# Optimization experiments

Measured on AMD Instinct MI355X. Metric: run time of the kernel, lower is better.

Reference implementation:

```python
import jax, jax.numpy as jnp
import numpy as np

T, N, L_DIM, P_DIM = 8192, 4096, 64, 32
IN_DIM = 3 * L_DIM  # library = [identity, square, sin]
MIN_TEMP, ALPHA, REP_COEF = 0.01, 0.999, 0.1


def build_library(X):
    # (T, L) -> (T, 3L): concatenated library features
    return jnp.concatenate([X, X * X, jnp.sin(X)], axis=1)


def setup_inputs() -> dict:
    key = jax.random.key(0)
    k = jax.random.split(key, 8)
    u = jax.random.uniform(k[6], (P_DIM, IN_DIM), minval=1e-7, maxval=1.0)
    return {
        "X_tilde_t_batch": jax.random.normal(k[0], (T, L_DIM), jnp.float32),
        "X_train_t_batch": jax.random.normal(k[1], (T, N), jnp.float32),
        "Y_train_t_batch": jax.random.normal(k[2], (T, N), jnp.float32),
        "temp": jnp.ones((1,), jnp.float32),
        "phi_bar_t": jax.random.normal(k[3], (P_DIM, L_DIM), jnp.float32) * 0.01,
        # spectral radius ~0.9 so the 8192-step linear recurrence stays bounded
        "A_tilde": jax.random.normal(k[4], (L_DIM, L_DIM), jnp.float32) * (0.9 / np.sqrt(L_DIM)),
        "U_l": jax.random.normal(k[5], (N, L_DIM), jnp.float32) / np.sqrt(N),
        "logits": jax.random.normal(k[7], (P_DIM, IN_DIM), jnp.float32),
        "gumbel_g": -jnp.log(-jnp.log(u)),  # Gumbel(0,1) noise, precomputed
    }


def reference(X_tilde_t_batch, X_train_t_batch, Y_train_t_batch, temp,
              phi_bar_t, A_tilde, U_l, logits, gumbel_g):
    # --- GumbelSelector (train=True) ---
    X_mod = build_library(X_tilde_t_batch)                           # (T, 3L)
    new_temp = jnp.maximum(MIN_TEMP, temp[0] * ALPHA)
    soft = jax.nn.softmax((logits + gumbel_g) / new_temp, axis=-1)   # (P, 3L)
    X_sel = X_mod @ soft.T                                           # (T, P) -- computed but unused downstream, as in source
    selected_idx = jnp.argmax(logits, axis=-1)                       # (P,)
    probs = jax.nn.softmax(logits, axis=-1)
    l0_pen = REP_COEF * jnp.sum(jnp.max(probs, axis=-1))             # computed, unused (as in source)

    # --- reconstruction_error: sequential linear state-space recurrence ---
    x0 = X_train_t_batch[0]                                          # (N,)  first column of X_train_batch
    xh0 = U_l.T @ x0                                                 # (L,)  projected initial state
    phi_bar = phi_bar_t.T                                            # (L, P)

    def step(xh, _):
        mod_sel = jnp.take(xh, selected_idx, mode='clip')            # (P,) irregular gather (clip matches jit take)
        xh = A_tilde @ xh + phi_bar @ mod_sel                        # tiny matvecs
        return xh, xh

    _, xh_seq = jax.lax.scan(step, xh0, None, length=T)              # (T, L)
    X_rec = xh_seq @ U_l.T                                           # (T, N) == (U_r @ xh_seq.T).T with U_r = U_l
    # Frobenius norm is transpose-invariant, so compute in (T, N) layout
    err = jnp.linalg.norm(Y_train_t_batch - X_rec) / jnp.linalg.norm(Y_train_t_batch)
    return (X_rec, err, new_temp, selected_idx)
```

## Files before the change

### kernel.cpp

```cpp
#include <hip/hip_runtime.h>
#include <math.h>

#define T_DIM 8192
#define N_DIM 4096
#define L 64
#define P 32
#define IN_DIM 192
#define S_CHUNK 16
#define N_CHUNK (T_DIM / S_CHUNK)
#define LDST 68

using f32x4   = __attribute__((ext_vector_type(4))) float;
using bf16x8  = __attribute__((ext_vector_type(8))) short;
using ushort8 = __attribute__((ext_vector_type(8))) unsigned short;

__device__ __forceinline__ unsigned short f2bf(float x) {
  unsigned u = __float_as_uint(x);
  u += 0x7fffu + ((u >> 16) & 1u);
  return (unsigned short)(u >> 16);
}
__device__ __forceinline__ float bf2f(unsigned short h) {
  return __uint_as_float(((unsigned)h) << 16);
}

__global__ __launch_bounds__(64) void k_xh0_part(const float* __restrict__ U,
                                                 const float* __restrict__ Xtr,
                                                 float* __restrict__ part,
                                                 double* __restrict__ acc) {
  int b = blockIdx.x;
  int l = threadIdx.x;
  if (b == 0 && l < 2) acc[l] = 0.0;
  int n0 = b * 64;
  float s = 0.f;
  #pragma unroll 8
  for (int i = 0; i < 64; ++i) {
    float x = Xtr[n0 + i];
    s += U[(size_t)(n0 + i) * L + l] * x;
  }
  part[b * 64 + l] = s;
}

__global__ __launch_bounds__(256) void k_usplit(const float* __restrict__ U,
                                                unsigned short* __restrict__ uh,
                                                unsigned short* __restrict__ ul) {
  int i = blockIdx.x * 256 + threadIdx.x;
  float4 x = ((const float4*)U)[i];
  ushort4 h, lo;
  h.x = f2bf(x.x); lo.x = f2bf(x.x - bf2f(h.x));
  h.y = f2bf(x.y); lo.y = f2bf(x.y - bf2f(h.y));
  h.z = f2bf(x.z); lo.z = f2bf(x.z - bf2f(h.z));
  h.w = f2bf(x.w); lo.w = f2bf(x.w - bf2f(h.w));
  ((ushort4*)uh)[i] = h;
  ((ushort4*)ul)[i] = lo;
}

__global__ __launch_bounds__(256, 1) void k_prep(const float* __restrict__ A_tilde,
                                                 const float* __restrict__ phi_bar_t,
                                                 const float* __restrict__ logits,
                                                 const float* __restrict__ temp,
                                                 const float* __restrict__ part,
                                                 float* __restrict__ Wm,
                                                 float* __restrict__ xh0,
                                                 float* __restrict__ out_tail) {
  __shared__ float buf[2][64 * LDST];
  __shared__ float sphi[P * L];
  __shared__ float spart[4 * 64];
  __shared__ int   sel_s[P];
  int tid = threadIdx.x;

  #pragma unroll
  for (int i = 0; i < 4; ++i) {
    int f = tid + 256 * i;
    int r = f >> 4, q = f & 15;
    float4 v = ((const float4*)A_tilde)[f];
    *(float4*)(buf[0] + r * LDST + q * 4) = v;
  }
  #pragma unroll
  for (int i = 0; i < 2; ++i) {
    int f = tid + 256 * i;
    ((float4*)sphi)[f] = ((const float4*)phi_bar_t)[f];
  }
  {
    int l = tid & 63, q = tid >> 6;
    float s = 0.f;
    #pragma unroll
    for (int i = 0; i < 16; ++i)
      s += part[(q * 16 + i) * 64 + l];
    spart[q * 64 + l] = s;
  }
  {
    int p = tid >> 3, d = tid & 7;
    const float* row = logits + p * IN_DIM;
    float best = -1e30f; int bk = 0;
    #pragma unroll
    for (int j = 0; j < 6; ++j) {
      int kb = (j * 8 + d) * 4;
      float4 v = *(const float4*)(row + kb);
      if (v.x > best) { best = v.x; bk = kb; }
      if (v.y > best) { best = v.y; bk = kb + 1; }
      if (v.z > best) { best = v.z; bk = kb + 2; }
      if (v.w > best) { best = v.w; bk = kb + 3; }
    }
    #pragma unroll
    for (int off = 4; off > 0; off >>= 1) {
      float vo = __shfl_down(best, off, 8);
      int   ko = __shfl_down(bk,   off, 8);
      if (vo > best || (vo == best && ko < bk)) { best = vo; bk = ko; }
    }
    if (d == 0) {
      sel_s[p] = bk;
      out_tail[2 + p] = (float)bk;
    }
  }
  if (tid == 255) out_tail[1] = fmaxf(0.01f, temp[0] * 0.999f);
  __syncthreads();

  if (tid < L) {
    #pragma unroll 4
    for (int p = 0; p < P; ++p) {
      int kk = sel_s[p]; if (kk > L - 1) kk = L - 1;
      buf[0][tid * LDST + kk] += sphi[p * L + tid];
    }
  } else if (tid < 128) {
    int l = tid - 64;
    xh0[l] = spart[l] + spart[64 + l] + spart[128 + l] + spart[192 + l];
  }
  __syncthreads();

  #pragma unroll
  for (int i = 0; i < 4; ++i) {
    int f = tid + 256 * i;
    int r = f >> 4, q = f & 15;
    *(float4*)(Wm + r * 64 + q * 4) = *(const float4*)(buf[0] + r * LDST + q * 4);
  }

  int r0 = (tid >> 4) << 2;
  int c0 = (tid & 15) << 2;
  int cur = 0;
  for (int j = 1; j <= 12; ++j) {
    const float* S = buf[cur];
    float* D = buf[cur ^ 1];
    float acc[4][4];
    #pragma unroll
    for (int i = 0; i < 4; ++i)
      #pragma unroll
      for (int c = 0; c < 4; ++c) acc[i][c] = 0.f;

    #pragma unroll
    for (int kb = 0; kb < 64; kb += 16) {
      float a[4][16];
      #pragma unroll
      for (int i = 0; i < 4; ++i)
        #pragma unroll
        for (int q = 0; q < 4; ++q) {
          float4 t4 = *(const float4*)(S + (r0 + i) * LDST + kb + q * 4);
          a[i][q * 4 + 0] = t4.x; a[i][q * 4 + 1] = t4.y;
          a[i][q * 4 + 2] = t4.z; a[i][q * 4 + 3] = t4.w;
        }
      #pragma unroll
      for (int kk = 0; kk < 16; ++kk) {
        float4 b4 = *(const float4*)(S + (kb + kk) * LDST + c0);
        #pragma unroll
        for (int i = 0; i < 4; ++i) {
          acc[i][0] += a[i][kk] * b4.x;
          acc[i][1] += a[i][kk] * b4.y;
          acc[i][2] += a[i][kk] * b4.z;
          acc[i][3] += a[i][kk] * b4.w;
        }
      }
    }
    #pragma unroll
    for (int i = 0; i < 4; ++i) {
      float4 o = {acc[i][0], acc[i][1], acc[i][2], acc[i][3]};
      *(float4*)(D + (r0 + i) * LDST + c0) = o;
      *(float4*)(Wm + j * 4096 + (r0 + i) * 64 + c0) = o;
    }
    __syncthreads();
    cur ^= 1;
  }
}

__global__ __launch_bounds__(64) void k_states(const float* __restrict__ Wm,
                                               const float* __restrict__ xh0,
                                               unsigned short* __restrict__ xhi,
                                               unsigned short* __restrict__ xlo) {
  int c = blockIdx.x;
  int l = threadIdx.x;
  float v = xh0[l];
  int e = c << 4;
  for (int j = 4; j <= 12; ++j) {
    if ((e >> j) & 1) {
      const float* W = Wm + j * 4096;
      float n0 = 0.f, n1 = 0.f, n2 = 0.f, n3 = 0.f;
      #pragma unroll
      for (int k = 0; k < 64; k += 4) {
        n0 += W[l * 64 + k]     * __shfl(v, k, 64);
        n1 += W[l * 64 + k + 1] * __shfl(v, k + 1, 64);
        n2 += W[l * 64 + k + 2] * __shfl(v, k + 2, 64);
        n3 += W[l * 64 + k + 3] * __shfl(v, k + 3, 64);
      }
      v = (n0 + n1) + (n2 + n3);
    }
  }
  float m[64];
  #pragma unroll
  for (int k = 0; k < 64; ++k) m[k] = Wm[l * 64 + k];
  int t0 = c * S_CHUNK;
  for (int i = 0; i < S_CHUNK; ++i) {
    float n0 = 0.f, n1 = 0.f, n2 = 0.f, n3 = 0.f;
    #pragma unroll
    for (int k = 0; k < 64; k += 4) {
      n0 += m[k]     * __shfl(v, k, 64);
      n1 += m[k + 1] * __shfl(v, k + 1, 64);
      n2 += m[k + 2] * __shfl(v, k + 2, 64);
      n3 += m[k + 3] * __shfl(v, k + 3, 64);
    }
    v = (n0 + n1) + (n2 + n3);
    unsigned short h = f2bf(v);
    unsigned short lo = f2bf(v - bf2f(h));
    size_t base = (size_t)(t0 + i) * L + l;
    xhi[base] = h; xlo[base] = lo;
  }
}

__global__ __launch_bounds__(256, 2) void k_xrec(const unsigned short* __restrict__ xhi,
                                                 const unsigned short* __restrict__ xlo,
                                                 const unsigned short* __restrict__ uh,
                                                 const unsigned short* __restrict__ ul,
                                                 const float* __restrict__ Y,
                                                 float* __restrict__ Xrec,
                                                 double* __restrict__ acc_g) {
  __shared__ __align__(16) unsigned short Xs[128 * 128];
  __shared__ __align__(16) unsigned short Us[128 * 128];
  __shared__ float red[512];

  int tid = threadIdx.x;
  int nt = blockIdx.x & 31, tt = blockIdx.x >> 5;
  int n0 = nt * 128, t0 = tt * 128;

  #pragma unroll
  for (int i = 0; i < 8; ++i) {
    int c = tid + 256 * i;
    int t = c >> 4, p = c & 15;
    const ushort8* src = (p < 8)
      ? (const ushort8*)(xhi + (size_t)(t0 + t) * L + p * 8)
      : (const ushort8*)(xlo + (size_t)(t0 + t) * L + (p - 8) * 8);
    *(ushort8*)((char*)Xs + t * 256 + ((p * 16) ^ ((t & 7) << 4))) = *src;
  }
  #pragma unroll
  for (int i = 0; i < 8; ++i) {
    int c = tid + 256 * i;
    int nn = c >> 4, p = c & 15;
    const ushort8* src = (p < 8)
      ? (const ushort8*)(uh + (size_t)(n0 + nn) * L + p * 8)
      : (const ushort8*)(ul + (size_t)(n0 + nn) * L + (p - 8) * 8);
    *(ushort8*)((char*)Us + nn * 256 + ((p * 16) ^ ((nn & 7) << 4))) = *src;
  }
  __syncthreads();

  int l = tid & 63, wid = tid >> 6;
  int wr = wid >> 1, wc = wid & 1;
  int lr = l & 15, lg = l >> 4;

  f32x4 acc[4][4];
  #pragma unroll
  for (int m = 0; m < 4; ++m)
    #pragma unroll
    for (int nf = 0; nf < 4; ++nf) acc[m][nf] = (f32x4){0.f, 0.f, 0.f, 0.f};

  const int KA[6] = {0, 32, 64, 96, 0, 32};
  const int KB[6] = {0, 32, 0, 32, 64, 96};
  #pragma unroll
  for (int s = 0; s < 6; ++s) {
    bf16x8 af[4], bfr[4];
    #pragma unroll
    for (int m = 0; m < 4; ++m) {
      int t_loc = wr * 64 + m * 16 + lr;
      int kk = KA[s] + lg * 8;
      af[m] = *(const bf16x8*)((const char*)Xs + t_loc * 256 + ((kk * 2) ^ ((t_loc & 7) << 4)));
    }
    #pragma unroll
    for (int nf = 0; nf < 4; ++nf) {
      int n_loc = wc * 64 + nf * 16 + lr;
      int kk = KB[s] + lg * 8;
      bfr[nf] = *(const bf16x8*)((const char*)Us + n_loc * 256 + ((kk * 2) ^ ((n_loc & 7) << 4)));
    }
    #pragma unroll
    for (int m = 0; m < 4; ++m)
      #pragma unroll
      for (int nf = 0; nf < 4; ++nf)
        acc[m][nf] = __builtin_amdgcn_mfma_f32_16x16x32_bf16(bfr[nf], af[m], acc[m][nf], 0, 0, 0);
  }

  float sd = 0.f, sy = 0.f;
  #pragma unroll
  for (int m = 0; m < 4; ++m) {
    #pragma unroll
    for (int nf = 0; nf < 4; ++nf) {
      int t = t0 + wr * 64 + m * 16 + lr;
      int n = n0 + wc * 64 + nf * 16 + lg * 4;
      size_t idx = (size_t)t * N_DIM + n;
      float4 y = *(const float4*)(Y + idx);
      f32x4 v = acc[m][nf];
      float d;
      d = y.x - v[0]; sd += d * d; sy += y.x * y.x;
      d = y.y - v[1]; sd += d * d; sy += y.y * y.y;
      d = y.z - v[2]; sd += d * d; sy += y.z * y.z;
      d = y.w - v[3]; sd += d * d; sy += y.w * y.w;
      *(float4*)(Xrec + idx) = (float4){v[0], v[1], v[2], v[3]};
    }
  }

  red[tid] = sd; red[256 + tid] = sy;
  __syncthreads();
  for (int s2 = 128; s2 > 0; s2 >>= 1) {
    if (tid < s2) { red[tid] += red[tid + s2]; red[256 + tid] += red[256 + tid + s2]; }
    __syncthreads();
  }
  if (tid == 0) {
    atomicAdd(acc_g,     (double)red[0]);
    atomicAdd(acc_g + 1, (double)red[256]);
  }
}

__global__ void k_err(const double* __restrict__ acc, float* __restrict__ out_tail) {
  out_tail[0] = (float)sqrt(acc[0] / acc[1]);
}

extern "C" void kernel_launch(void* const* d_in, const int* in_sizes, int n_in,
                              void* d_out, int out_size, void* d_ws, size_t ws_size,
                              hipStream_t stream) {
  const float* X_train = (const float*)d_in[1];
  const float* Y       = (const float*)d_in[2];
  const float* temp    = (const float*)d_in[3];
  const float* phi     = (const float*)d_in[4];
  const float* A_tilde = (const float*)d_in[5];
  const float* U       = (const float*)d_in[6];
  const float* logits  = (const float*)d_in[7];
  float* out = (float*)d_out;
  float* out_tail = out + (size_t)T_DIM * N_DIM;

  char* w = (char*)d_ws;
  double* acc          = (double*)w;
  float* Wm            = (float*)(w + 64);
  float* xh0           = (float*)(w + 213056);
  float* part          = (float*)(w + 213312);
  unsigned short* uh   = (unsigned short*)(w + 262144);
  unsigned short* ul   = (unsigned short*)(w + 786432);
  unsigned short* xhi  = (unsigned short*)(w + 1310720);
  unsigned short* xlo  = (unsigned short*)(w + 2359296);

  k_xh0_part<<<64, 64, 0, stream>>>(U, X_train, part, acc);
  k_usplit<<<(N_DIM * L / 4) / 256, 256, 0, stream>>>(U, uh, ul);
  k_prep<<<1, 256, 0, stream>>>(A_tilde, phi, logits, temp, part, Wm, xh0, out_tail);
  k_states<<<N_CHUNK, 64, 0, stream>>>(Wm, xh0, xhi, xlo);
  k_xrec<<<2048, 256, 0, stream>>>(xhi, xlo, uh, ul, Y, out, acc);
  k_err<<<1, 1, 0, stream>>>(acc, out_tail);
}
```

Measured before the change: 128.0 us.

## Pre-pack bf16 hi/lo operands in MFMA fragment order and drop LDS staging

The U split and state kernels now write the hi/lo bf16 operands directly in MFMA fragment order (16-row tiles, lane-contiguous 8-element groups). The reconstruction GEMM can then load fragments straight from global memory instead of staging swizzled tiles in shared memory behind a barrier. The LDS footprint shrinks, so the launch bound is raised to 3 blocks per CU, and X_rec is written with nontemporal stores. The trade-off is redundant global/L2 fragment loads across waves and blocks in place of shared-memory reuse.

Result: no change. 128.4 us (+0.3%).

```diff
diff --git a/kernel.cpp b/kernel.cpp
--- a/kernel.cpp
+++ b/kernel.cpp
@@ -21,6 +21,11 @@
 }
 __device__ __forceinline__ float bf2f(unsigned short h) {
   return __uint_as_float(((unsigned)h) << 16);
+}
+
+__device__ __forceinline__ bf16x8 ldfrag(const unsigned short* __restrict__ base,
+                                         int tile16, int gb, int lg, int lr) {
+  return *(const bf16x8*)(base + ((size_t)((tile16 * 16 + gb + lg) * 16 + lr)) * 8);
 }
 
 __global__ __launch_bounds__(64) void k_xh0_part(const float* __restrict__ U,
@@ -41,17 +46,21 @@
 }
 
 __global__ __launch_bounds__(256) void k_usplit(const float* __restrict__ U,
-                                                unsigned short* __restrict__ uh,
-                                                unsigned short* __restrict__ ul) {
-  int i = blockIdx.x * 256 + threadIdx.x;
-  float4 x = ((const float4*)U)[i];
-  ushort4 h, lo;
-  h.x = f2bf(x.x); lo.x = f2bf(x.x - bf2f(h.x));
-  h.y = f2bf(x.y); lo.y = f2bf(x.y - bf2f(h.y));
-  h.z = f2bf(x.z); lo.z = f2bf(x.z - bf2f(h.z));
-  h.w = f2bf(x.w); lo.w = f2bf(x.w - bf2f(h.w));
-  ((ushort4*)uh)[i] = h;
-  ((ushort4*)ul)[i] = lo;
+                                                unsigned short* __restrict__ upk) {
+  int idx = blockIdx.x * 256 + threadIdx.x;
+  int lr = idx & 15, g = (idx >> 4) & 15, nn16 = idx >> 8;
+  int n = nn16 * 16 + lr;
+  int k0 = (g & 7) * 8;
+  float4 a = *(const float4*)(U + (size_t)n * L + k0);
+  float4 b = *(const float4*)(U + (size_t)n * L + k0 + 4);
+  ushort8 o;
+  float v[8] = {a.x, a.y, a.z, a.w, b.x, b.y, b.z, b.w};
+  #pragma unroll
+  for (int j = 0; j < 8; ++j) {
+    unsigned short h = f2bf(v[j]);
+    o[j] = (g < 8) ? h : f2bf(v[j] - bf2f(h));
+  }
+  *(ushort8*)(upk + (size_t)idx * 8) = o;
 }
 
 __global__ __launch_bounds__(256, 1) void k_prep(const float* __restrict__ A_tilde,
@@ -182,8 +191,8 @@
 
 __global__ __launch_bounds__(64) void k_states(const float* __restrict__ Wm,
                                                const float* __restrict__ xh0,
-                                               unsigned short* __restrict__ xhi,
-                                               unsigned short* __restrict__ xlo) {
+                                               unsigned short* __restrict__ xpk) {
+  __shared__ float sx[16 * LDST];
   int c = blockIdx.x;
   int l = threadIdx.x;
   float v = xh0[l];
@@ -205,7 +214,6 @@
   float m[64];
   #pragma unroll
   for (int k = 0; k < 64; ++k) m[k] = Wm[l * 64 + k];
-  int t0 = c * S_CHUNK;
   for (int i = 0; i < S_CHUNK; ++i) {
     float n0 = 0.f, n1 = 0.f, n2 = 0.f, n3 = 0.f;
     #pragma unroll
@@ -216,81 +224,107 @@
       n3 += m[k + 3] * __shfl(v, k + 3, 64);
     }
     v = (n0 + n1) + (n2 + n3);
-    unsigned short h = f2bf(v);
-    unsigned short lo = f2bf(v - bf2f(h));
-    size_t base = (size_t)(t0 + i) * L + l;
-    xhi[base] = h; xlo[base] = lo;
-  }
-}
-
-__global__ __launch_bounds__(256, 2) void k_xrec(const unsigned short* __restrict__ xhi,
-                                                 const unsigned short* __restrict__ xlo,
-                                                 const unsigned short* __restrict__ uh,
-                                                 const unsigned short* __restrict__ ul,
+    sx[i * LDST + l] = v;
+  }
+  __syncthreads();
+
+  #pragma unroll
+  for (int it = 0; it < 4; ++it) {
+    int idx = l + 64 * it;
+    int lr = idx & 15, g = idx >> 4;
+    int k0 = (g & 7) * 8;
+    float4 a = *(const float4*)(sx + lr * LDST + k0);
+    float4 b = *(const float4*)(sx + lr * LDST + k0 + 4);
+    float vv[8] = {a.x, a.y, a.z, a.w, b.x, b.y, b.z, b.w};
+    ushort8 o;
+    #pragma unroll
+    for (int j = 0; j < 8; ++j) {
+      unsigned short h = f2bf(vv[j]);
+      o[j] = (g < 8) ? h : f2bf(vv[j] - bf2f(h));
+    }
+    *(ushort8*)(xpk + ((size_t)c * 256 + idx) * 8) = o;
+  }
+}
+
+__global__ __launch_bounds__(256, 3) void k_xrec(const unsigned short* __restrict__ xpk,
+                                                 const unsigned short* __restrict__ upk,
                                                  const float* __restrict__ Y,
                                                  float* __restrict__ Xrec,
                                                  double* __restrict__ acc_g) {
-  __shared__ __align__(16) unsigned short Xs[128 * 128];
-  __shared__ __align__(16) unsigned short Us[128 * 128];
   __shared__ float red[512];
 
   int tid = threadIdx.x;
   int nt = blockIdx.x & 31, tt = blockIdx.x >> 5;
   int n0 = nt * 128, t0 = tt * 128;
 
-  #pragma unroll
-  for (int i = 0; i < 8; ++i) {
-    int c = tid + 256 * i;
-    int t = c >> 4, p = c & 15;
-    const ushort8* src = (p < 8)
-      ? (const ushort8*)(xhi + (size_t)(t0 + t) * L + p * 8)
-      : (const ushort8*)(xlo + (size_t)(t0 + t) * L + (p - 8) * 8);
-    *(ushort8*)((char*)Xs + t * 256 + ((p * 16) ^ ((t & 7) << 4))) = *src;
-  }
-  #pragma unroll
-  for (int i = 0; i < 8; ++i) {
-    int c = tid + 256 * i;
-    int nn = c >> 4, p = c & 15;
-    const ushort8* src = (p < 8)
-      ? (const ushort8*)(uh + (size_t)(n0 + nn) * L + p * 8)
-      : (const ushort8*)(ul + (size_t)(n0 + nn) * L + (p - 8) * 8);
-    *(ushort8*)((char*)Us + nn * 256 + ((p * 16) ^ ((nn & 7) << 4))) = *src;
-  }
-  __syncthreads();
-
   int l = tid & 63, wid = tid >> 6;
   int wr = wid >> 1, wc = wid & 1;
   int lr = l & 15, lg = l >> 4;
 
+  int xt = (t0 >> 4) + wr * 4;
+  int un = (n0 >> 4) + wc * 4;
+
   f32x4 acc[4][4];
   #pragma unroll
   for (int m = 0; m < 4; ++m)
     #pragma unroll
     for (int nf = 0; nf < 4; ++nf) acc[m][nf] = (f32x4){0.f, 0.f, 0.f, 0.f};
 
-  const int KA[6] = {0, 32, 64, 96, 0, 32};
-  const int KB[6] = {0, 32, 0, 32, 64, 96};
-  #pragma unroll
-  for (int s = 0; s < 6; ++s) {
-    bf16x8 af[4], bfr[4];
-    #pragma unroll
-    for (int m = 0; m < 4; ++m) {
-      int t_loc = wr * 64 + m * 16 + lr;
-      int kk = KA[s] + lg * 8;
-      af[m] = *(const bf16x8*)((const char*)Xs + t_loc * 256 + ((kk * 2) ^ ((t_loc & 7) << 4)));
-    }
-    #pragma unroll
-    for (int nf = 0; nf < 4; ++nf) {
-      int n_loc = wc * 64 + nf * 16 + lr;
-      int kk = KB[s] + lg * 8;
-      bfr[nf] = *(const bf16x8*)((const char*)Us + n_loc * 256 + ((kk * 2) ^ ((n_loc & 7) << 4)));
-    }
-    #pragma unroll
-    for (int m = 0; m < 4; ++m)
-      #pragma unroll
-      for (int nf = 0; nf < 4; ++nf)
-        acc[m][nf] = __builtin_amdgcn_mfma_f32_16x16x32_bf16(bfr[nf], af[m], acc[m][nf], 0, 0, 0);
-  }
+  bf16x8 af[4], bfr[4], bf2r[4];
+
+  #pragma unroll
+  for (int m = 0; m < 4; ++m)  af[m]   = ldfrag(xpk, xt + m, 0, lg, lr);
+  #pragma unroll
+  for (int nf = 0; nf < 4; ++nf) bfr[nf]  = ldfrag(upk, un + nf, 0, lg, lr);
+  #pragma unroll
+  for (int nf = 0; nf < 4; ++nf) bf2r[nf] = ldfrag(upk, un + nf, 8, lg, lr);
+  #pragma unroll
+  for (int m = 0; m < 4; ++m)
+    #pragma unroll
+    for (int nf = 0; nf < 4; ++nf)
+      acc[m][nf] = __builtin_amdgcn_mfma_f32_16x16x32_bf16(bfr[nf], af[m], acc[m][nf], 0, 0, 0);
+  #pragma unroll
+  for (int m = 0; m < 4; ++m)
+    #pragma unroll
+    for (int nf = 0; nf < 4; ++nf)
+      acc[m][nf] = __builtin_amdgcn_mfma_f32_16x16x32_bf16(bf2r[nf], af[m], acc[m][nf], 0, 0, 0);
+
+  #pragma unroll
+  for (int m = 0; m < 4; ++m)  af[m]   = ldfrag(xpk, xt + m, 4, lg, lr);
+  #pragma unroll
+  for (int nf = 0; nf < 4; ++nf) bfr[nf]  = ldfrag(upk, un + nf, 4, lg, lr);
+  #pragma unroll
+  for (int nf = 0; nf < 4; ++nf) bf2r[nf] = ldfrag(upk, un + nf, 12, lg, lr);
+  #pragma unroll
+  for (int m = 0; m < 4; ++m)
+    #pragma unroll
+    for (int nf = 0; nf < 4; ++nf)
+      acc[m][nf] = __builtin_amdgcn_mfma_f32_16x16x32_bf16(bfr[nf], af[m], acc[m][nf], 0, 0, 0);
+  #pragma unroll
+  for (int m = 0; m < 4; ++m)
+    #pragma unroll
+    for (int nf = 0; nf < 4; ++nf)
+      acc[m][nf] = __builtin_amdgcn_mfma_f32_16x16x32_bf16(bf2r[nf], af[m], acc[m][nf], 0, 0, 0);
+
+  #pragma unroll
+  for (int m = 0; m < 4; ++m)  af[m]  = ldfrag(xpk, xt + m, 8, lg, lr);
+  #pragma unroll
+  for (int nf = 0; nf < 4; ++nf) bfr[nf] = ldfrag(upk, un + nf, 0, lg, lr);
+  #pragma unroll
+  for (int m = 0; m < 4; ++m)
+    #pragma unroll
+    for (int nf = 0; nf < 4; ++nf)
+      acc[m][nf] = __builtin_amdgcn_mfma_f32_16x16x32_bf16(bfr[nf], af[m], acc[m][nf], 0, 0, 0);
+
+  #pragma unroll
+  for (int m = 0; m < 4; ++m)  af[m]  = ldfrag(xpk, xt + m, 12, lg, lr);
+  #pragma unroll
+  for (int nf = 0; nf < 4; ++nf) bfr[nf] = ldfrag(upk, un + nf, 4, lg, lr);
+  #pragma unroll
+  for (int m = 0; m < 4; ++m)
+    #pragma unroll
+    for (int nf = 0; nf < 4; ++nf)
+      acc[m][nf] = __builtin_amdgcn_mfma_f32_16x16x32_bf16(bfr[nf], af[m], acc[m][nf], 0, 0, 0);
 
   float sd = 0.f, sy = 0.f;
   #pragma unroll
@@ -307,7 +341,7 @@
       d = y.y - v[1]; sd += d * d; sy += y.y * y.y;
       d = y.z - v[2]; sd += d * d; sy += y.z * y.z;
       d = y.w - v[3]; sd += d * d; sy += y.w * y.w;
-      *(float4*)(Xrec + idx) = (float4){v[0], v[1], v[2], v[3]};
+      __builtin_nontemporal_store(v, (f32x4*)(Xrec + idx));
     }
   }
 
@@ -345,15 +379,13 @@
   float* Wm            = (float*)(w + 64);
   float* xh0           = (float*)(w + 213056);
   float* part          = (float*)(w + 213312);
-  unsigned short* uh   = (unsigned short*)(w + 262144);
-  unsigned short* ul   = (unsigned short*)(w + 786432);
-  unsigned short* xhi  = (unsigned short*)(w + 1310720);
-  unsigned short* xlo  = (unsigned short*)(w + 2359296);
+  unsigned short* upk  = (unsigned short*)(w + 262144);
+  unsigned short* xpk  = (unsigned short*)(w + 1310720);
 
   k_xh0_part<<<64, 64, 0, stream>>>(U, X_train, part, acc);
-  k_usplit<<<(N_DIM * L / 4) / 256, 256, 0, stream>>>(U, uh, ul);
+  k_usplit<<<(N_DIM / 16), 256, 0, stream>>>(U, upk);
   k_prep<<<1, 256, 0, stream>>>(A_tilde, phi, logits, temp, part, Wm, xh0, out_tail);
-  k_states<<<N_CHUNK, 64, 0, stream>>>(Wm, xh0, xhi, xlo);
-  k_xrec<<<2048, 256, 0, stream>>>(xhi, xlo, uh, ul, Y, out, acc);
+  k_states<<<N_CHUNK, 64, 0, stream>>>(Wm, xh0, xpk);
+  k_xrec<<<2048, 256, 0, stream>>>(xpk, upk, Y, out, acc);
   k_err<<<1, 1, 0, stream>>>(acc, out_tail);
 }
```
